# Optimization experiments

Measured on AMD Instinct MI355X. Metric: run time of the kernel, lower is better.

The kernel has to match this reference:

```python
import jax, jax.numpy as jnp
import numpy as np

IN_FEATURES = 4096
OUT_FEATURES = 4096
RANK = 16
SCALING = 1.0  # lora_alpha / r = 16 / 16


def setup_inputs() -> dict:
    key = jax.random.key(0)
    k1, k2, k3, k4 = jax.random.split(key, 4)
    x = jax.random.normal(k1, (4, 2048, IN_FEATURES), dtype=jnp.float32)
    # packed weight: (out_features, in_features // 4), repeated x4 at forward time
    weight_packed = jax.random.normal(k2, (OUT_FEATURES, IN_FEATURES // 4), dtype=jnp.float32) * 0.02
    lora_A = jax.random.normal(k3, (RANK, IN_FEATURES), dtype=jnp.float32) * 0.02
    lora_B = jax.random.normal(k4, (OUT_FEATURES, RANK), dtype=jnp.float32) * 0.02
    return {"x": x, "weight_packed": weight_packed, "lora_A": lora_A, "lora_B": lora_B, "scaling": 1}


def reference(x, weight_packed, lora_A, lora_B, scaling):
    W = jnp.tile(weight_packed, (1, 4))  # [out, in]
    base = jnp.einsum('bsi,oi->bso', x, W)
    # LoRA low-rank path: (x @ A^T) @ B^T * scaling
    lora = jnp.einsum('bsr,or->bso', jnp.einsum('bsi,ri->bsr', x, lora_A), lora_B)
    return base + lora * jnp.float32(scaling)
```

## Files before the change

kernel.cpp:

```cpp
#include <hip/hip_runtime.h>
#include <hip/hip_bf16.h>
#include <stdint.h>

#define M_DIM 8192
#define N_DIM 4096
#define K_DIM 4096
#define RANK  16

#define BM 256
#define BN 256
#define BK 64
#define NKT (K_DIM / BK)

typedef __attribute__((ext_vector_type(8))) __bf16 bf16x8;
typedef __attribute__((ext_vector_type(4))) float  f32x4;
typedef __attribute__((ext_vector_type(8))) unsigned short u16x8;

__device__ __forceinline__ unsigned short f2bf(float f) {
    union { float f; uint32_t u; } c; c.f = f;
    uint32_t b = c.u;
    b += 0x7FFFu + ((b >> 16) & 1u);
    return (unsigned short)(b >> 16);
}

#define WEFF_BLOCKS 1024
#define CONV_BLOCKS 2048
__global__ __launch_bounds__(256) void prep_kernel(
    const float* __restrict__ x,
    const float* __restrict__ wp,
    const float* __restrict__ lA,
    const float* __restrict__ lB,
    const int*   __restrict__ scaling,
    unsigned short* __restrict__ xb,
    unsigned short* __restrict__ weff) {
    __shared__ float lAs[16][512];
    const int t = threadIdx.x;
    if (blockIdx.x < WEFF_BLOCKS) {
        const int bo = blockIdx.x >> 3;
        const int bi = blockIdx.x & 7;
#pragma unroll
        for (int v = 0; v < 8; ++v) {
            int idx = v * 256 + t;
            int r = idx >> 7;
            int c4 = idx & 127;
            reinterpret_cast<float4*>(&lAs[r][0])[c4] =
                reinterpret_cast<const float4*>(lA + (size_t)r * 4096 + bi * 512)[c4];
        }
        __syncthreads();
        const int row = t >> 3;
        const int o = bo * 32 + row;
        const float s = (float)scaling[0];
        float b[RANK];
#pragma unroll
        for (int r = 0; r < RANK; ++r) b[r] = lB[o * RANK + r] * s;
        const float* wrow = wp + (size_t)o * 1024;
        const int cbase = (t & 7) * 4;
#pragma unroll
        for (int j = 0; j < 16; ++j) {
            int c = cbase + j * 32;
            int gi = bi * 512 + c;
            float4 w = *reinterpret_cast<const float4*>(wrow + (gi & 1023));
            float a0 = w.x, a1 = w.y, a2 = w.z, a3 = w.w;
#pragma unroll
            for (int r = 0; r < RANK; ++r) {
                float4 la = *reinterpret_cast<const float4*>(&lAs[r][c]);
                a0 = fmaf(b[r], la.x, a0);
                a1 = fmaf(b[r], la.y, a1);
                a2 = fmaf(b[r], la.z, a2);
                a3 = fmaf(b[r], la.w, a3);
            }
            ushort4 ov;
            ov.x = f2bf(a0); ov.y = f2bf(a1); ov.z = f2bf(a2); ov.w = f2bf(a3);
            *reinterpret_cast<ushort4*>(weff + (size_t)o * 4096 + gi) = ov;
        }
    } else {
        const int n8 = (M_DIM * K_DIM) / 8;
        int idx = (blockIdx.x - WEFF_BLOCKS) * 256 + t;
        const int stride = CONV_BLOCKS * 256;
        for (int i = idx; i < n8; i += stride) {
            float4 v0 = reinterpret_cast<const float4*>(x)[2 * i];
            float4 v1 = reinterpret_cast<const float4*>(x)[2 * i + 1];
            u16x8 o;
            o[0] = f2bf(v0.x); o[1] = f2bf(v0.y); o[2] = f2bf(v0.z); o[3] = f2bf(v0.w);
            o[4] = f2bf(v1.x); o[5] = f2bf(v1.y); o[6] = f2bf(v1.z); o[7] = f2bf(v1.w);
            reinterpret_cast<u16x8*>(xb)[i] = o;
        }
    }
}


template<int MH, int NH>
__device__ __forceinline__ void mfma_quad(const bf16x8 (&a)[4][2], const bf16x8 (&b)[2][2],
                                          f32x4 (&acc)[8][4]) {
#pragma unroll
    for (int kc = 0; kc < 2; ++kc)
#pragma unroll
        for (int mf = 0; mf < 4; ++mf)
#pragma unroll
            for (int nf = 0; nf < 2; ++nf)
                acc[MH * 4 + mf][NH * 2 + nf] = __builtin_amdgcn_mfma_f32_16x16x32_bf16(
                    a[mf][kc], b[nf][kc], acc[MH * 4 + mf][NH * 2 + nf], 0, 0, 0);
}

__global__ __launch_bounds__(512, 2) void gemm_kernel(
    const unsigned short* __restrict__ A,
    const unsigned short* __restrict__ B,
    float* __restrict__ C)
{
    __shared__ __align__(16) char lds[131072];

    const int tid  = threadIdx.x;
    const int lane = tid & 63;
    const int wave = tid >> 6;
    const int wr = wave >> 2;
    const int wc = wave & 3;

    const int bid = blockIdx.x;
    const int swz = (bid & 7) * 64 + (bid >> 3);
    const int bm = swz >> 4;
    const int bn = swz & 15;
    const int m0 = bm * BM;
    const int n0 = bn * BN;

    const int srccol = 8 * ((tid & 7) ^ ((tid >> 3) & 7));
    const int wub    = (tid & ~63) * 16;
    const unsigned short* Ag = A + (size_t)(m0 + (tid >> 3)) * K_DIM + srccol;
    const unsigned short* Bg = B + (size_t)(n0 + (tid >> 8) * 64 + ((tid >> 3) & 31)) * K_DIM + srccol;

#define STAGE_A(buf, mh, kt) do { \
    __builtin_amdgcn_global_load_lds( \
        (const __attribute__((address_space(1))) void*)(Ag + (size_t)((mh) * 64) * K_DIM + (size_t)(kt) * 64), \
        (__attribute__((address_space(3))) void*)(lds + (buf) * 65536 + (mh) * 16384 + wub), 16, 0, 0); \
    __builtin_amdgcn_global_load_lds( \
        (const __attribute__((address_space(1))) void*)(Ag + (size_t)(128 + (mh) * 64) * K_DIM + (size_t)(kt) * 64), \
        (__attribute__((address_space(3))) void*)(lds + (buf) * 65536 + (mh) * 16384 + 8192 + wub), 16, 0, 0); \
} while (0)

#define STAGE_B(buf, nh, kt) do { \
    __builtin_amdgcn_global_load_lds( \
        (const __attribute__((address_space(1))) void*)(Bg + (size_t)((nh) * 32) * K_DIM + (size_t)(kt) * 64), \
        (__attribute__((address_space(3))) void*)(lds + (buf) * 65536 + 32768 + (nh) * 16384 + wub), 16, 0, 0); \
    __builtin_amdgcn_global_load_lds( \
        (const __attribute__((address_space(1))) void*)(Bg + (size_t)(128 + (nh) * 32) * K_DIM + (size_t)(kt) * 64), \
        (__attribute__((address_space(3))) void*)(lds + (buf) * 65536 + 32768 + (nh) * 16384 + 8192 + wub), 16, 0, 0); \
} while (0)

    const int wrA   = wr * 8192;
    const int wcB   = wc * 4096;
    const int rdrow = (lane & 15) * 128;
    const int rdxor = (lane & 7) << 4;
    const int rdg   = (lane >> 4) * 16;

#define RD_A(dst, buf, mh) do { \
    _Pragma("unroll") for (int mf = 0; mf < 4; ++mf) \
    _Pragma("unroll") for (int kc = 0; kc < 2; ++kc) \
        dst[mf][kc] = *(const bf16x8*)(lds + (buf) * 65536 + (mh) * 16384 + wrA + rdrow + mf * 2048 + ((kc * 64 + rdg) ^ rdxor)); \
} while (0)

#define RD_B(dst, buf, nh) do { \
    _Pragma("unroll") for (int nf = 0; nf < 2; ++nf) \
    _Pragma("unroll") for (int kc = 0; kc < 2; ++kc) \
        dst[nf][kc] = *(const bf16x8*)(lds + (buf) * 65536 + 32768 + (nh) * 16384 + wcB + rdrow + nf * 2048 + ((kc * 64 + rdg) ^ rdxor)); \
} while (0)

#define PH_TAIL(QUAD) \
    __builtin_amdgcn_s_barrier(); \
    asm volatile("s_waitcnt lgkmcnt(0)" ::: "memory"); \
    __builtin_amdgcn_s_setprio(1); \
    QUAD; \
    __builtin_amdgcn_s_setprio(0);

    f32x4 acc[8][4];
#pragma unroll
    for (int i = 0; i < 8; ++i)
#pragma unroll
        for (int j = 0; j < 4; ++j) acc[i][j] = (f32x4){0.f, 0.f, 0.f, 0.f};

    bf16x8 afr[4][2];
    bf16x8 bfr[2][2];

    STAGE_A(0, 0, 0); STAGE_B(0, 1, 0); STAGE_A(0, 1, 0); STAGE_B(0, 0, 0);
    STAGE_A(1, 0, 1); STAGE_B(1, 1, 1);
    asm volatile("s_waitcnt vmcnt(4)" ::: "memory");
    __builtin_amdgcn_s_barrier();

    for (int it = 0; it < NKT / 2; ++it) {
        const int k1 = 2 * it + 1;
        const int k2 = (2 * it + 2) & (NKT - 1);
        const int k3 = (2 * it + 3) & (NKT - 1);

        RD_A(afr, 0, 0); RD_B(bfr, 0, 0);
        STAGE_A(1, 1, k1);
        asm volatile("s_waitcnt lgkmcnt(8)" ::: "memory");
        PH_TAIL((mfma_quad<0, 0>(afr, bfr, acc)));
        __builtin_amdgcn_s_barrier();
        RD_B(bfr, 0, 1);
        STAGE_B(1, 0, k1);
        PH_TAIL((mfma_quad<0, 1>(afr, bfr, acc)));
        __builtin_amdgcn_s_barrier();
        RD_A(afr, 0, 1);
        STAGE_A(0, 0, k2);
        PH_TAIL((mfma_quad<1, 1>(afr, bfr, acc)));
        __builtin_amdgcn_s_barrier();
        RD_B(bfr, 0, 0);
        STAGE_B(0, 1, k2);
        PH_TAIL((mfma_quad<1, 0>(afr, bfr, acc)));
        asm volatile("s_waitcnt vmcnt(4)" ::: "memory");
        __builtin_amdgcn_s_barrier();
        RD_A(afr, 1, 0); RD_B(bfr, 1, 0);
        STAGE_A(0, 1, k2);
        asm volatile("s_waitcnt lgkmcnt(8)" ::: "memory");
        PH_TAIL((mfma_quad<0, 0>(afr, bfr, acc)));
        __builtin_amdgcn_s_barrier();
        RD_B(bfr, 1, 1);
        STAGE_B(0, 0, k2);
        PH_TAIL((mfma_quad<0, 1>(afr, bfr, acc)));
        __builtin_amdgcn_s_barrier();
        RD_A(afr, 1, 1);
        STAGE_A(1, 0, k3);
        PH_TAIL((mfma_quad<1, 1>(afr, bfr, acc)));
        __builtin_amdgcn_s_barrier();
        RD_B(bfr, 1, 0);
        STAGE_B(1, 1, k3);
        PH_TAIL((mfma_quad<1, 0>(afr, bfr, acc)));
        asm volatile("s_waitcnt vmcnt(4)" ::: "memory");
        __builtin_amdgcn_s_barrier();
    }

    const int crow = m0 + wr * 128 + (lane >> 4) * 4;
    const int ccol = n0 + wc * 64 + (lane & 15);
#pragma unroll
    for (int mi = 0; mi < 8; ++mi)
#pragma unroll
        for (int ni = 0; ni < 4; ++ni)
#pragma unroll
            for (int r = 0; r < 4; ++r)
                C[(size_t)(crow + mi * 16 + r) * N_DIM + ccol + ni * 16] = acc[mi][ni][r];

#undef STAGE_A
#undef STAGE_B
#undef RD_A
#undef RD_B
#undef PH_TAIL
}

extern "C" void kernel_launch(void* const* d_in, const int* in_sizes, int n_in,
                              void* d_out, int out_size, void* d_ws, size_t ws_size,
                              hipStream_t stream) {
    const float* x  = (const float*)d_in[0];
    const float* wp = (const float*)d_in[1];
    const float* lA = (const float*)d_in[2];
    const float* lB = (const float*)d_in[3];
    const int*   sc = (const int*)d_in[4];
    float* out = (float*)d_out;

    unsigned short* xb   = (unsigned short*)d_ws;
    unsigned short* weff = (unsigned short*)d_ws + (size_t)M_DIM * K_DIM;

    prep_kernel<<<WEFF_BLOCKS + CONV_BLOCKS, 256, 0, stream>>>(x, wp, lA, lB, sc, xb, weff);

    int grid = (M_DIM / BM) * (N_DIM / BN);
    gemm_kernel<<<grid, 512, 0, stream>>>(xb, weff, out);
}
```

Measured before the change: 282.8 us.

## Double-buffer B fragments to drop phase barriers and stage epilogue through LDS

Splits the B register fragment into two buffers, so successive MFMA phases no longer overwrite fragments other phases still need. This lets most of the intra-iteration s_barrier calls be removed. The epilogue now writes accumulators into a per-wave LDS scratch tile and reads them back as 16-byte vectors for coalesced global stores, replacing scattered scalar stores. Launch bounds drop to one block per SM so the extra fragment registers fit. The risks are LDS races from the fewer barriers, in-flight staging loads overlapping the epilogue scratch area, and higher register pressure.

```diff
diff --git a/kernel.cpp b/kernel.cpp
--- a/kernel.cpp
+++ b/kernel.cpp
@@ -102,7 +102,7 @@
                     a[mf][kc], b[nf][kc], acc[MH * 4 + mf][NH * 2 + nf], 0, 0, 0);
 }
 
-__global__ __launch_bounds__(512, 2) void gemm_kernel(
+__global__ __launch_bounds__(512, 1) void gemm_kernel(
     const unsigned short* __restrict__ A,
     const unsigned short* __restrict__ B,
     float* __restrict__ C)
@@ -177,7 +177,7 @@
         for (int j = 0; j < 4; ++j) acc[i][j] = (f32x4){0.f, 0.f, 0.f, 0.f};
 
     bf16x8 afr[4][2];
-    bf16x8 bfr[2][2];
+    bf16x8 b0[2][2], b1[2][2];
 
     STAGE_A(0, 0, 0); STAGE_B(0, 1, 0); STAGE_A(0, 1, 0); STAGE_B(0, 0, 0);
     STAGE_A(1, 0, 1); STAGE_B(1, 1, 1);
@@ -189,53 +189,63 @@
         const int k2 = (2 * it + 2) & (NKT - 1);
         const int k3 = (2 * it + 3) & (NKT - 1);
 
-        RD_A(afr, 0, 0); RD_B(bfr, 0, 0);
+        RD_A(afr, 0, 0); RD_B(b0, 0, 0);
         STAGE_A(1, 1, k1);
         asm volatile("s_waitcnt lgkmcnt(8)" ::: "memory");
-        PH_TAIL((mfma_quad<0, 0>(afr, bfr, acc)));
-        __builtin_amdgcn_s_barrier();
-        RD_B(bfr, 0, 1);
+        PH_TAIL((mfma_quad<0, 0>(afr, b0, acc)));
+        RD_B(b1, 0, 1);
         STAGE_B(1, 0, k1);
-        PH_TAIL((mfma_quad<0, 1>(afr, bfr, acc)));
-        __builtin_amdgcn_s_barrier();
+        PH_TAIL((mfma_quad<0, 1>(afr, b1, acc)));
         RD_A(afr, 0, 1);
         STAGE_A(0, 0, k2);
-        PH_TAIL((mfma_quad<1, 1>(afr, bfr, acc)));
-        __builtin_amdgcn_s_barrier();
-        RD_B(bfr, 0, 0);
+        PH_TAIL((mfma_quad<1, 1>(afr, b1, acc)));
         STAGE_B(0, 1, k2);
-        PH_TAIL((mfma_quad<1, 0>(afr, bfr, acc)));
+        PH_TAIL((mfma_quad<1, 0>(afr, b0, acc)));
         asm volatile("s_waitcnt vmcnt(4)" ::: "memory");
         __builtin_amdgcn_s_barrier();
-        RD_A(afr, 1, 0); RD_B(bfr, 1, 0);
+        RD_A(afr, 1, 0); RD_B(b0, 1, 0);
         STAGE_A(0, 1, k2);
         asm volatile("s_waitcnt lgkmcnt(8)" ::: "memory");
-        PH_TAIL((mfma_quad<0, 0>(afr, bfr, acc)));
-        __builtin_amdgcn_s_barrier();
-        RD_B(bfr, 1, 1);
+        PH_TAIL((mfma_quad<0, 0>(afr, b0, acc)));
+        RD_B(b1, 1, 1);
         STAGE_B(0, 0, k2);
-        PH_TAIL((mfma_quad<0, 1>(afr, bfr, acc)));
-        __builtin_amdgcn_s_barrier();
+        PH_TAIL((mfma_quad<0, 1>(afr, b1, acc)));
         RD_A(afr, 1, 1);
         STAGE_A(1, 0, k3);
-        PH_TAIL((mfma_quad<1, 1>(afr, bfr, acc)));
-        __builtin_amdgcn_s_barrier();
-        RD_B(bfr, 1, 0);
+        PH_TAIL((mfma_quad<1, 1>(afr, b1, acc)));
         STAGE_B(1, 1, k3);
-        PH_TAIL((mfma_quad<1, 0>(afr, bfr, acc)));
+        PH_TAIL((mfma_quad<1, 0>(afr, b0, acc)));
         asm volatile("s_waitcnt vmcnt(4)" ::: "memory");
         __builtin_amdgcn_s_barrier();
     }
 
-    const int crow = m0 + wr * 128 + (lane >> 4) * 4;
-    const int ccol = n0 + wc * 64 + (lane & 15);
-#pragma unroll
-    for (int mi = 0; mi < 8; ++mi)
-#pragma unroll
-        for (int ni = 0; ni < 4; ++ni)
-#pragma unroll
-            for (int r = 0; r < 4; ++r)
-                C[(size_t)(crow + mi * 16 + r) * N_DIM + ccol + ni * 16] = acc[mi][ni][r];
+    {
+        float* lsc = (float*)lds + wave * (16 * 84);
+        const int wcol  = lane & 15;
+        const int wrow4 = (lane >> 4) * 4;
+        const int rrow  = lane >> 3;
+        const int rcol  = (lane & 7) * 4;
+        const int crow0 = m0 + wr * 128;
+        const int ccol0 = n0 + wc * 64;
+#pragma unroll
+        for (int mi = 0; mi < 8; ++mi) {
+#pragma unroll
+            for (int ni = 0; ni < 4; ++ni)
+#pragma unroll
+                for (int r = 0; r < 4; ++r)
+                    lsc[(wrow4 + r) * 84 + ni * 16 + wcol] = acc[mi][ni][r];
+            asm volatile("s_waitcnt lgkmcnt(0)" ::: "memory");
+#pragma unroll
+            for (int rh = 0; rh < 2; ++rh)
+#pragma unroll
+                for (int j = 0; j < 2; ++j) {
+                    f32x4 v = *(const f32x4*)&lsc[(rh * 8 + rrow) * 84 + rcol + j * 32];
+                    *(f32x4*)&C[(size_t)(crow0 + mi * 16 + rh * 8 + rrow) * N_DIM +
+                                ccol0 + rcol + j * 32] = v;
+                }
+            asm volatile("s_waitcnt lgkmcnt(0)" ::: "memory");
+        }
+    }
 
 #undef STAGE_A
 #undef STAGE_B
```

Measured after the change: 271.2 us. 4.1% less time.

## Double-buffer B fragments and reorder LDS staging to avoid B re-reads

Applied to the files above, without the earlier changes.

Keeps two B fragment register sets (b0, b1) so the fourth MFMA quad reuses the first B fragment instead of re-reading it from LDS, removing one LDS read group per half-iteration. The global-to-LDS staging order is reshuffled so the next tile's A and B halves are issued earlier, and the vmcnt wait changes from 4 to 6. Launch bounds drop to one block per CU to free registers for the extra fragments, which may reduce latency hiding from co-resident blocks.

```diff
diff --git a/kernel.cpp b/kernel.cpp
--- a/kernel.cpp
+++ b/kernel.cpp
@@ -102,7 +102,7 @@
                     a[mf][kc], b[nf][kc], acc[MH * 4 + mf][NH * 2 + nf], 0, 0, 0);
 }
 
-__global__ __launch_bounds__(512, 2) void gemm_kernel(
+__global__ __launch_bounds__(512, 1) void gemm_kernel(
     const unsigned short* __restrict__ A,
     const unsigned short* __restrict__ B,
     float* __restrict__ C)
@@ -163,12 +163,22 @@
         dst[nf][kc] = *(const bf16x8*)(lds + (buf) * 65536 + 32768 + (nh) * 16384 + wcB + rdrow + nf * 2048 + ((kc * 64 + rdg) ^ rdxor)); \
 } while (0)
 
-#define PH_TAIL(QUAD) \
+#define PH(QUAD) \
     __builtin_amdgcn_s_barrier(); \
     asm volatile("s_waitcnt lgkmcnt(0)" ::: "memory"); \
     __builtin_amdgcn_s_setprio(1); \
     QUAD; \
-    __builtin_amdgcn_s_setprio(0);
+    __builtin_amdgcn_s_setprio(0); \
+    __builtin_amdgcn_s_barrier();
+
+#define PH_V(QUAD) \
+    __builtin_amdgcn_s_barrier(); \
+    asm volatile("s_waitcnt lgkmcnt(0)" ::: "memory"); \
+    __builtin_amdgcn_s_setprio(1); \
+    QUAD; \
+    __builtin_amdgcn_s_setprio(0); \
+    asm volatile("s_waitcnt vmcnt(6)" ::: "memory"); \
+    __builtin_amdgcn_s_barrier();
 
     f32x4 acc[8][4];
 #pragma unroll
@@ -177,54 +187,42 @@
         for (int j = 0; j < 4; ++j) acc[i][j] = (f32x4){0.f, 0.f, 0.f, 0.f};
 
     bf16x8 afr[4][2];
-    bf16x8 bfr[2][2];
-
-    STAGE_A(0, 0, 0); STAGE_B(0, 1, 0); STAGE_A(0, 1, 0); STAGE_B(0, 0, 0);
-    STAGE_A(1, 0, 1); STAGE_B(1, 1, 1);
-    asm volatile("s_waitcnt vmcnt(4)" ::: "memory");
+    bf16x8 b0[2][2], b1[2][2];
+
+    STAGE_A(0, 0, 0); STAGE_B(0, 0, 0); STAGE_B(0, 1, 0); STAGE_A(0, 1, 0);
+    STAGE_A(1, 0, 1); STAGE_B(1, 0, 1); STAGE_B(1, 1, 1);
+    asm volatile("s_waitcnt vmcnt(6)" ::: "memory");
     __builtin_amdgcn_s_barrier();
 
     for (int it = 0; it < NKT / 2; ++it) {
-        const int k1 = 2 * it + 1;
-        const int k2 = (2 * it + 2) & (NKT - 1);
-        const int k3 = (2 * it + 3) & (NKT - 1);
-
-        RD_A(afr, 0, 0); RD_B(bfr, 0, 0);
-        STAGE_A(1, 1, k1);
+        const int o  = 2 * it + 1;
+        const int e2 = (2 * it + 2) & (NKT - 1);
+        const int o2 = (2 * it + 3) & (NKT - 1);
+
+        RD_A(afr, 0, 0); RD_B(b0, 0, 0);
+        STAGE_A(1, 1, o);
         asm volatile("s_waitcnt lgkmcnt(8)" ::: "memory");
-        PH_TAIL((mfma_quad<0, 0>(afr, bfr, acc)));
-        __builtin_amdgcn_s_barrier();
-        RD_B(bfr, 0, 1);
-        STAGE_B(1, 0, k1);
-        PH_TAIL((mfma_quad<0, 1>(afr, bfr, acc)));
-        __builtin_amdgcn_s_barrier();
+        PH((mfma_quad<0, 0>(afr, b0, acc)));
+        RD_B(b1, 0, 1);
+        STAGE_A(0, 0, e2);
+        PH((mfma_quad<0, 1>(afr, b1, acc)));
         RD_A(afr, 0, 1);
-        STAGE_A(0, 0, k2);
-        PH_TAIL((mfma_quad<1, 1>(afr, bfr, acc)));
-        __builtin_amdgcn_s_barrier();
-        RD_B(bfr, 0, 0);
-        STAGE_B(0, 1, k2);
-        PH_TAIL((mfma_quad<1, 0>(afr, bfr, acc)));
-        asm volatile("s_waitcnt vmcnt(4)" ::: "memory");
-        __builtin_amdgcn_s_barrier();
-        RD_A(afr, 1, 0); RD_B(bfr, 1, 0);
-        STAGE_A(0, 1, k2);
+        STAGE_B(0, 0, e2);
+        PH((mfma_quad<1, 1>(afr, b1, acc)));
+        STAGE_B(0, 1, e2);
+        PH_V((mfma_quad<1, 0>(afr, b0, acc)));
+        RD_A(afr, 1, 0); RD_B(b0, 1, 0);
+        STAGE_A(0, 1, e2);
         asm volatile("s_waitcnt lgkmcnt(8)" ::: "memory");
-        PH_TAIL((mfma_quad<0, 0>(afr, bfr, acc)));
-        __builtin_amdgcn_s_barrier();
-        RD_B(bfr, 1, 1);
-        STAGE_B(0, 0, k2);
-        PH_TAIL((mfma_quad<0, 1>(afr, bfr, acc)));
-        __builtin_amdgcn_s_barrier();
+        PH((mfma_quad<0, 0>(afr, b0, acc)));
+        RD_B(b1, 1, 1);
+        STAGE_A(1, 0, o2);
+        PH((mfma_quad<0, 1>(afr, b1, acc)));
         RD_A(afr, 1, 1);
-        STAGE_A(1, 0, k3);
-        PH_TAIL((mfma_quad<1, 1>(afr, bfr, acc)));
-        __builtin_amdgcn_s_barrier();
-        RD_B(bfr, 1, 0);
-        STAGE_B(1, 1, k3);
-        PH_TAIL((mfma_quad<1, 0>(afr, bfr, acc)));
-        asm volatile("s_waitcnt vmcnt(4)" ::: "memory");
-        __builtin_amdgcn_s_barrier();
+        STAGE_B(1, 0, o2);
+        PH((mfma_quad<1, 1>(afr, b1, acc)));
+        STAGE_B(1, 1, o2);
+        PH_V((mfma_quad<1, 0>(afr, b0, acc)));
     }
 
     const int crow = m0 + wr * 128 + (lane >> 4) * 4;
@@ -241,7 +239,8 @@
 #undef STAGE_B
 #undef RD_A
 #undef RD_B
-#undef PH_TAIL
+#undef PH
+#undef PH_V
 }
 
 extern "C" void kernel_launch(void* const* d_in, const int* in_sizes, int n_in,
```

Measured after the change: 279.8 us. About the same (-1.1%).
